# Kernel optimization log

Measured on AMD Instinct MI355X. Metric: run time of the kernel, lower is better.

Reference implementation:

```python
import jax, jax.numpy as jnp
import numpy as np

BS, N, D, H = 4, 2048, 512, 8
DK = D // H
XAVIER_STD = float(np.sqrt(2.0 / (D + D)))  # xavier_normal_, gain=1


def setup_inputs() -> dict:
    key = jax.random.key(0)
    ks = jax.random.split(key, 10)
    Q = jax.random.normal(ks[0], (BS, N, D), jnp.float32)
    K = jax.random.normal(ks[1], (BS, N, D), jnp.float32)
    V = jax.random.normal(ks[2], (BS, N, D), jnp.float32)
    q_mas = jax.random.randint(ks[3], (BS, N, 1), 0, 2).astype(jnp.float32)
    k_mas = jax.random.randint(ks[4], (BS, N, 1), 0, 2).astype(jnp.float32)
    # 0/1 attention mask; force self-edges so no row is fully masked (avoids NaN softmax)
    att_mas = jax.random.randint(ks[5], (BS, N, N), 0, 2).astype(jnp.float32)
    att_mas = jnp.maximum(att_mas, jnp.eye(N, dtype=jnp.float32)[None])
    WQ = jax.random.normal(ks[6], (D, D), jnp.float32) * XAVIER_STD
    WK = jax.random.normal(ks[7], (D, D), jnp.float32) * XAVIER_STD
    WV = jax.random.normal(ks[8], (D, D), jnp.float32) * XAVIER_STD
    WO = jax.random.normal(ks[9], (D, D), jnp.float32) * XAVIER_STD
    return {"Q": Q, "K": K, "V": V, "q_mas": q_mas, "k_mas": k_mas,
            "att_mas": att_mas, "WQ": WQ, "WK": WK, "WV": WV, "WO": WO}


def reference(Q, K, V, q_mas, k_mas, att_mas, WQ, WK, WV, WO):
    bs, n, d = Q.shape
    h, dk = H, DK
    qm = q_mas.reshape(bs, 1, n, 1)  # (bs,1,n,1)
    km = k_mas.reshape(bs, 1, n, 1)
    # nn.Linear (no bias): x @ W.T ; split heads -> (bs,h,n,dk); apply pre-masks
    Qh = qm * (Q @ WQ.T).reshape(bs, n, h, dk).transpose(0, 2, 1, 3)
    Kh = km * (K @ WK.T).reshape(bs, n, h, dk).transpose(0, 2, 1, 3)
    Vh = km * (V @ WV.T).reshape(bs, n, h, dk).transpose(0, 2, 1, 3)
    scores = jnp.einsum('bhqd,bhkd->bhqk', Qh, Kh) / jnp.sqrt(jnp.float32(dk))
    mas = att_mas.reshape(bs, 1, n, n)
    scores = jnp.where(mas.astype(bool), scores, -jnp.inf)
    attn = jax.nn.softmax(scores, axis=-1) * mas
    y = jnp.einsum('bhqk,bhkd->bhqd', attn, Vh) * km  # post-mask (note: km over query dim, as in source)
    y = y.transpose(0, 2, 1, 3).reshape(bs, n, d)
    y = (y @ WO.T) * k_mas.reshape(bs, n, 1)
    return y
```

## Files before the change

kernel.cpp:

```cpp
#include <hip/hip_runtime.h>


#define BS_    4
#define NSEQ   2048
#define DMODEL 512
#define NH     8
#define DKH    64
#define MROWS  (BS_ * NSEQ)

typedef unsigned short ushort_t;
typedef __attribute__((ext_vector_type(8))) short short8;
typedef __attribute__((ext_vector_type(4))) float floatx4;

__device__ __forceinline__ ushort_t f2bf(float f) {
    unsigned int x = __builtin_bit_cast(unsigned int, f);
    unsigned int lsb = (x >> 16) & 1u;
    x += 0x7fffu + lsb;
    return (ushort_t)(x >> 16);
}
__device__ __forceinline__ floatx4 mfma_bf16(short8 a, short8 b, floatx4 c) {
    return __builtin_amdgcn_mfma_f32_16x16x32_bf16(a, b, c, 0, 0, 0);
}
__device__ __forceinline__ void gld16(const ushort_t* g, ushort_t* l) {
    __builtin_amdgcn_global_load_lds(
        (const __attribute__((address_space(1))) unsigned int*)g,
        (__attribute__((address_space(3))) unsigned int*)l, 16, 0, 0);
}

__global__ __launch_bounds__(256) void cvt3_kernel(const float* __restrict__ a,
                                                   const float* __restrict__ b,
                                                   const float* __restrict__ c,
                                                   ushort_t* __restrict__ dst, int n4) {
    const float* src = (blockIdx.y == 0) ? a : (blockIdx.y == 1) ? b : c;
    ushort_t* d = dst + (size_t)blockIdx.y * ((size_t)n4 * 4);
    const int i = blockIdx.x * blockDim.x + threadIdx.x;
    const float4 v = ((const float4*)src)[i];
    ushort4 o;
    o.x = f2bf(v.x); o.y = f2bf(v.y); o.z = f2bf(v.z); o.w = f2bf(v.w);
    ((ushort4*)d)[i] = o;
}

__global__ __launch_bounds__(256) void cvt4_kernel(const float* __restrict__ a,
                                                   const float* __restrict__ b,
                                                   const float* __restrict__ c,
                                                   const float* __restrict__ e,
                                                   ushort_t* __restrict__ dst, int n4) {
    const float* src = (blockIdx.y == 0) ? a : (blockIdx.y == 1) ? b
                     : (blockIdx.y == 2) ? c : e;
    ushort_t* d = dst + (size_t)blockIdx.y * ((size_t)n4 * 4);
    const int i = blockIdx.x * blockDim.x + threadIdx.x;
    const float4 v = ((const float4*)src)[i];
    ushort4 o;
    o.x = f2bf(v.x); o.y = f2bf(v.y); o.z = f2bf(v.z); o.w = f2bf(v.w);
    ((ushort4*)d)[i] = o;
}

__global__ __launch_bounds__(256) void gemm_proj(const ushort_t* __restrict__ Xall,
                                                 const ushort_t* __restrict__ Wall,
                                                 const float* __restrict__ qmas,
                                                 const float* __restrict__ kmas,
                                                 ushort_t* __restrict__ Qh,
                                                 ushort_t* __restrict__ Kh,
                                                 ushort_t* __restrict__ Vt) {
    __shared__ ushort_t As[128 * 32];
    __shared__ ushort_t Bs[128 * 32];
    const int z = blockIdx.z;
    const ushort_t* X  = Xall + (size_t)z * MROWS * DMODEL;
    const ushort_t* Wb = Wall + (size_t)z * DMODEL * DMODEL;
    const float* rowmask = (z == 0) ? qmas : kmas;

    const int tid  = threadIdx.x;
    const int wave = tid >> 6;
    const int lane = tid & 63;
    const int l16  = lane & 15;
    const int quad = lane >> 4;
    const int wr   = wave >> 1;
    const int wc   = wave & 1;
    const int m0   = blockIdx.x * 128;
    const int n0   = blockIdx.y * 128;
    const int crow = lane >> 2;
    const int koff = (lane & 3) * 8;

    floatx4 acc[4][4];
#pragma unroll
    for (int t = 0; t < 4; ++t)
#pragma unroll
        for (int u = 0; u < 4; ++u) acc[t][u] = (floatx4){0.f, 0.f, 0.f, 0.f};

    for (int k0 = 0; k0 < DMODEL; k0 += 32) {
#pragma unroll
        for (int c2 = 0; c2 < 2; ++c2) {
            const int c = wave * 2 + c2;
            gld16(X  + (size_t)(m0 + c * 16 + crow) * DMODEL + k0 + koff, &As[c * 512]);
            gld16(Wb + (size_t)(n0 + c * 16 + crow) * DMODEL + k0 + koff, &Bs[c * 512]);
        }
        __syncthreads();
        short8 a[4], b[4];
#pragma unroll
        for (int t = 0; t < 4; ++t)
            a[t] = *(const short8*)&As[(wr * 64 + t * 16 + l16) * 32 + quad * 8];
#pragma unroll
        for (int u = 0; u < 4; ++u)
            b[u] = *(const short8*)&Bs[(wc * 64 + u * 16 + l16) * 32 + quad * 8];
#pragma unroll
        for (int t = 0; t < 4; ++t)
#pragma unroll
            for (int u = 0; u < 4; ++u) acc[t][u] = mfma_bf16(a[t], b[u], acc[t][u]);
        __syncthreads();
    }

    float rm[4][4];
#pragma unroll
    for (int t = 0; t < 4; ++t)
#pragma unroll
        for (int r = 0; r < 4; ++r)
            rm[t][r] = rowmask[m0 + wr * 64 + t * 16 + quad * 4 + r];

    const int bb    = m0 >> 11;
    const int nbase = (m0 & (NSEQ - 1)) + wr * 64;
#pragma unroll
    for (int t = 0; t < 4; ++t) {
#pragma unroll
        for (int u = 0; u < 4; ++u) {
            const int d = n0 + wc * 64 + u * 16 + l16;
            const int h = d >> 6, cc = d & 63;
            if (z < 2) {
                ushort_t* dst = (z == 0) ? Qh : Kh;
#pragma unroll
                for (int r = 0; r < 4; ++r) {
                    const int n = nbase + t * 16 + quad * 4 + r;
                    dst[((size_t)(bb * NH + h) * NSEQ + n) * DKH + cc] =
                        f2bf(acc[t][u][r] * rm[t][r]);
                }
            } else {
                ushort4 pk;
                pk.x = f2bf(acc[t][u][0] * rm[t][0]);
                pk.y = f2bf(acc[t][u][1] * rm[t][1]);
                pk.z = f2bf(acc[t][u][2] * rm[t][2]);
                pk.w = f2bf(acc[t][u][3] * rm[t][3]);
                const int n = nbase + t * 16 + quad * 4;
                *(ushort4*)(Vt + ((size_t)(bb * NH + h) * DKH + cc) * NSEQ + n) = pk;
            }
        }
    }
}

__global__ __launch_bounds__(256) void gemm_out(const ushort_t* __restrict__ X,
                                                const ushort_t* __restrict__ Wb,
                                                const float* __restrict__ rowmask,
                                                float* __restrict__ dst) {
    __shared__ ushort_t As[128 * 32];
    __shared__ ushort_t Bs[128 * 32];
    const int tid  = threadIdx.x;
    const int wave = tid >> 6;
    const int lane = tid & 63;
    const int l16  = lane & 15;
    const int quad = lane >> 4;
    const int wr   = wave >> 1;
    const int wc   = wave & 1;
    const int m0   = blockIdx.x * 128;
    const int n0   = blockIdx.y * 128;
    const int crow = lane >> 2;
    const int koff = (lane & 3) * 8;

    floatx4 acc[4][4];
#pragma unroll
    for (int t = 0; t < 4; ++t)
#pragma unroll
        for (int u = 0; u < 4; ++u) acc[t][u] = (floatx4){0.f, 0.f, 0.f, 0.f};

    for (int k0 = 0; k0 < DMODEL; k0 += 32) {
#pragma unroll
        for (int c2 = 0; c2 < 2; ++c2) {
            const int c = wave * 2 + c2;
            gld16(X  + (size_t)(m0 + c * 16 + crow) * DMODEL + k0 + koff, &As[c * 512]);
            gld16(Wb + (size_t)(n0 + c * 16 + crow) * DMODEL + k0 + koff, &Bs[c * 512]);
        }
        __syncthreads();
        short8 a[4], b[4];
#pragma unroll
        for (int t = 0; t < 4; ++t)
            a[t] = *(const short8*)&As[(wr * 64 + t * 16 + l16) * 32 + quad * 8];
#pragma unroll
        for (int u = 0; u < 4; ++u)
            b[u] = *(const short8*)&Bs[(wc * 64 + u * 16 + l16) * 32 + quad * 8];
#pragma unroll
        for (int t = 0; t < 4; ++t)
#pragma unroll
            for (int u = 0; u < 4; ++u) acc[t][u] = mfma_bf16(a[t], b[u], acc[t][u]);
        __syncthreads();
    }

#pragma unroll
    for (int t = 0; t < 4; ++t) {
#pragma unroll
        for (int r = 0; r < 4; ++r) {
            const int m = m0 + wr * 64 + t * 16 + quad * 4 + r;
            const float rm = rowmask[m];
#pragma unroll
            for (int u = 0; u < 4; ++u) {
                const int d = n0 + wc * 64 + u * 16 + l16;
                dst[(size_t)m * DMODEL + d] = acc[t][u][r] * rm;
            }
        }
    }
}

__global__ __launch_bounds__(256) void attn_kernel(const ushort_t* __restrict__ Qh,
                                                   const ushort_t* __restrict__ Kh,
                                                   const ushort_t* __restrict__ Vt,
                                                   const float* __restrict__ amas,
                                                   const float* __restrict__ kmas,
                                                   ushort_t* __restrict__ y) {
    __shared__ __align__(16) ushort_t Ks[128 * 72];
    __shared__ __align__(16) ushort_t Vs[64 * 136];
    __shared__ __align__(16) ushort_t Ps[4][16 * 136];

    const int tid  = threadIdx.x;
    const int wave = tid >> 6;
    const int lane = tid & 63;
    const int l16  = lane & 15;
    const int quad = lane >> 4;
    const int h    = blockIdx.y;
    const int b    = blockIdx.z;
    const int qw   = blockIdx.x * 64 + wave * 16;

    const ushort_t* Kb = Kh + (size_t)(b * NH + h) * NSEQ * DKH;
    const ushort_t* Vb = Vt + (size_t)(b * NH + h) * DKH * NSEQ;
    const float*    Am = amas + (size_t)(b * NSEQ + qw) * NSEQ;

    const ushort_t* Qp = Qh + ((size_t)((b * NH + h) * NSEQ) + qw + l16) * DKH + quad * 8;
    const short8 qfa = *(const short8*)Qp;
    const short8 qfb = *(const short8*)(Qp + 32);

    float lpart[4] = {0.f, 0.f, 0.f, 0.f};
    floatx4 accO[4];
#pragma unroll
    for (int ct = 0; ct < 4; ++ct) accO[ct] = (floatx4){0.f, 0.f, 0.f, 0.f};

    const float CEXP = 0.18033688011112042f;

    for (int kt = 0; kt < NSEQ / 128; ++kt) {
        const int k0 = kt * 128;

        short8 kv[4], vv[4];
#pragma unroll
        for (int i = 0; i < 4; ++i) {
            const int c = tid + i * 256;
            kv[i] = *(const short8*)(Kb + (size_t)(k0 + (c >> 3)) * DKH + (c & 7) * 8);
        }
#pragma unroll
        for (int i = 0; i < 4; ++i) {
            const int c = tid + i * 256;
            vv[i] = *(const short8*)(Vb + (size_t)(c >> 4) * NSEQ + k0 + (c & 15) * 8);
        }
        float av[8][4];
#pragma unroll
        for (int fr = 0; fr < 8; ++fr)
#pragma unroll
            for (int r = 0; r < 4; ++r)
                av[fr][r] = Am[(size_t)(quad * 4 + r) * NSEQ + k0 + fr * 16 + l16];

        __syncthreads();
#pragma unroll
        for (int i = 0; i < 4; ++i) {
            const int c = tid + i * 256;
            *(short8*)&Ks[(c >> 3) * 72 + (c & 7) * 8] = kv[i];
        }
#pragma unroll
        for (int i = 0; i < 4; ++i) {
            const int c = tid + i * 256;
            *(short8*)&Vs[(c >> 4) * 136 + (c & 15) * 8] = vv[i];
        }
        __syncthreads();

        floatx4 S[8];
#pragma unroll
        for (int fr = 0; fr < 8; ++fr) {
            const short8 ka = *(const short8*)&Ks[(fr * 16 + l16) * 72 + quad * 8];
            const short8 kb = *(const short8*)&Ks[(fr * 16 + l16) * 72 + 32 + quad * 8];
            floatx4 s = {0.f, 0.f, 0.f, 0.f};
            s = mfma_bf16(qfa, ka, s);
            s = mfma_bf16(qfb, kb, s);
            S[fr] = s;
        }

#pragma unroll
        for (int fr = 0; fr < 8; ++fr) {
#pragma unroll
            for (int r = 0; r < 4; ++r) {
                const float p = av[fr][r] * exp2f(S[fr][r] * CEXP);
                lpart[r] += p;
                Ps[wave][(quad * 4 + r) * 136 + fr * 16 + l16] = f2bf(p);
            }
        }

        __builtin_amdgcn_wave_barrier();
        short8 pf[4];
#pragma unroll
        for (int kf = 0; kf < 4; ++kf)
            pf[kf] = *(const short8*)&Ps[wave][l16 * 136 + kf * 32 + quad * 8];
        __builtin_amdgcn_wave_barrier();

#pragma unroll
        for (int ct = 0; ct < 4; ++ct) {
#pragma unroll
            for (int kf = 0; kf < 4; ++kf) {
                const short8 vb = *(const short8*)&Vs[(ct * 16 + l16) * 136 + kf * 32 + quad * 8];
                accO[ct] = mfma_bf16(pf[kf], vb, accO[ct]);
            }
        }
    }

#pragma unroll
    for (int r = 0; r < 4; ++r) {
        float l = lpart[r];
        l += __shfl_xor(l, 1);
        l += __shfl_xor(l, 2);
        l += __shfl_xor(l, 4);
        l += __shfl_xor(l, 8);
        const int q = qw + quad * 4 + r;
        const float scale = kmas[b * NSEQ + q] / l;
#pragma unroll
        for (int ct = 0; ct < 4; ++ct) {
            y[(size_t)(b * NSEQ + q) * DMODEL + h * DKH + ct * 16 + l16] =
                f2bf(accO[ct][r] * scale);
        }
    }
}

extern "C" void kernel_launch(void* const* d_in, const int* in_sizes, int n_in,
                              void* d_out, int out_size, void* d_ws, size_t ws_size,
                              hipStream_t stream) {
    (void)in_sizes; (void)n_in; (void)out_size; (void)ws_size;
    const float* Q  = (const float*)d_in[0];
    const float* K  = (const float*)d_in[1];
    const float* V  = (const float*)d_in[2];
    const float* qm = (const float*)d_in[3];
    const float* km = (const float*)d_in[4];
    const float* am = (const float*)d_in[5];
    const float* WQ = (const float*)d_in[6];
    const float* WK = (const float*)d_in[7];
    const float* WV = (const float*)d_in[8];
    const float* WO = (const float*)d_in[9];

    const size_t XN = (size_t)MROWS * DMODEL;
    const size_t WN = (size_t)DMODEL * DMODEL;
    ushort_t* Xbf = (ushort_t*)d_ws;
    ushort_t* Wbf = Xbf + 3 * XN;
    ushort_t* WOb = Wbf + 3 * WN;
    ushort_t* Qh  = Wbf + 4 * WN;
    ushort_t* Kh  = Qh + XN;
    ushort_t* Vt  = Kh + XN;
    ushort_t* y   = Vt + XN;
    float* out = (float*)d_out;

    hipLaunchKernelGGL(cvt3_kernel, dim3(4096, 3), dim3(256), 0, stream,
                       Q, K, V, Xbf, (int)(XN / 4));
    hipLaunchKernelGGL(cvt4_kernel, dim3(256, 4), dim3(256), 0, stream,
                       WQ, WK, WV, WO, Wbf, (int)(WN / 4));

    hipLaunchKernelGGL(gemm_proj, dim3(MROWS / 128, DMODEL / 128, 3), dim3(256), 0, stream,
                       Xbf, Wbf, qm, km, Qh, Kh, Vt);

    hipLaunchKernelGGL(attn_kernel, dim3(NSEQ / 64, NH, BS_), dim3(256), 0, stream,
                       Qh, Kh, Vt, am, km, y);

    hipLaunchKernelGGL(gemm_out, dim3(MROWS / 128, DMODEL / 128), dim3(256), 0, stream,
                       y, WOb, km, out);
}
```

Measured before the change: 288.4 us.

## Use direct-to-LDS loads in attention, read weights from global, widen GEMM K-step

The projection and output GEMMs now step K by 64 and stage only the activation tile in shared memory via global_load_lds, while each wave reads its weight fragments straight from global memory into registers. The attention kernel replaces register-staged K/V copies with direct global-to-LDS loads into unpadded 32-wide subtiles, re-lays out the P buffer to match, and sets a launch-bounds occupancy hint of 3. The bf16 conversion drops round-to-nearest-even tie handling for a cheaper round-half-up. These changes aim to cut LDS traffic, VGPR staging and barrier overhead, but unpadded LDS rows risk bank conflicts, and uncoalesced weight loads may add global latency.

```diff
diff --git a/kernel.cpp b/kernel.cpp
--- a/kernel.cpp
+++ b/kernel.cpp
@@ -14,9 +14,7 @@
 
 __device__ __forceinline__ ushort_t f2bf(float f) {
     unsigned int x = __builtin_bit_cast(unsigned int, f);
-    unsigned int lsb = (x >> 16) & 1u;
-    x += 0x7fffu + lsb;
-    return (ushort_t)(x >> 16);
+    return (ushort_t)((x + 0x8000u) >> 16);
 }
 __device__ __forceinline__ floatx4 mfma_bf16(short8 a, short8 b, floatx4 c) {
     return __builtin_amdgcn_mfma_f32_16x16x32_bf16(a, b, c, 0, 0, 0);
@@ -62,8 +60,7 @@
                                                  ushort_t* __restrict__ Qh,
                                                  ushort_t* __restrict__ Kh,
                                                  ushort_t* __restrict__ Vt) {
-    __shared__ ushort_t As[128 * 32];
-    __shared__ ushort_t Bs[128 * 32];
+    __shared__ ushort_t As[2][128 * 32];
     const int z = blockIdx.z;
     const ushort_t* X  = Xall + (size_t)z * MROWS * DMODEL;
     const ushort_t* Wb = Wall + (size_t)z * DMODEL * DMODEL;
@@ -78,8 +75,8 @@
     const int wc   = wave & 1;
     const int m0   = blockIdx.x * 128;
     const int n0   = blockIdx.y * 128;
-    const int crow = lane >> 2;
-    const int koff = (lane & 3) * 8;
+    const int r4   = lane >> 2;
+    const int p4   = lane & 3;
 
     floatx4 acc[4][4];
 #pragma unroll
@@ -87,25 +84,39 @@
 #pragma unroll
         for (int u = 0; u < 4; ++u) acc[t][u] = (floatx4){0.f, 0.f, 0.f, 0.f};
 
-    for (int k0 = 0; k0 < DMODEL; k0 += 32) {
-#pragma unroll
-        for (int c2 = 0; c2 < 2; ++c2) {
-            const int c = wave * 2 + c2;
-            gld16(X  + (size_t)(m0 + c * 16 + crow) * DMODEL + k0 + koff, &As[c * 512]);
-            gld16(Wb + (size_t)(n0 + c * 16 + crow) * DMODEL + k0 + koff, &Bs[c * 512]);
-        }
-        __syncthreads();
-        short8 a[4], b[4];
+    const ushort_t* Wrow[4];
+#pragma unroll
+    for (int u = 0; u < 4; ++u)
+        Wrow[u] = Wb + (size_t)(n0 + wc * 64 + u * 16 + l16) * DMODEL + quad * 8;
+
+    for (int k0 = 0; k0 < DMODEL; k0 += 64) {
+#pragma unroll
+        for (int i = 0; i < 4; ++i) {
+            const int idx = wave * 4 + i;
+            const int h = idx >> 3, rg = idx & 7;
+            gld16(X + (size_t)(m0 + rg * 16 + r4) * DMODEL + k0 + h * 32 + p4 * 8,
+                  &As[h][rg * 512]);
+        }
+        short8 bf[4][2];
+#pragma unroll
+        for (int u = 0; u < 4; ++u)
+#pragma unroll
+            for (int kc = 0; kc < 2; ++kc)
+                bf[u][kc] = *(const short8*)(Wrow[u] + k0 + kc * 32);
+        __syncthreads();
+        short8 af[4][2];
 #pragma unroll
         for (int t = 0; t < 4; ++t)
-            a[t] = *(const short8*)&As[(wr * 64 + t * 16 + l16) * 32 + quad * 8];
-#pragma unroll
-        for (int u = 0; u < 4; ++u)
-            b[u] = *(const short8*)&Bs[(wc * 64 + u * 16 + l16) * 32 + quad * 8];
+#pragma unroll
+            for (int kc = 0; kc < 2; ++kc)
+                af[t][kc] = *(const short8*)&As[kc][(wr * 64 + t * 16 + l16) * 32 + quad * 8];
 #pragma unroll
         for (int t = 0; t < 4; ++t)
 #pragma unroll
-            for (int u = 0; u < 4; ++u) acc[t][u] = mfma_bf16(a[t], b[u], acc[t][u]);
+            for (int u = 0; u < 4; ++u) {
+                acc[t][u] = mfma_bf16(af[t][0], bf[u][0], acc[t][u]);
+                acc[t][u] = mfma_bf16(af[t][1], bf[u][1], acc[t][u]);
+            }
         __syncthreads();
     }
 
@@ -149,8 +160,7 @@
                                                 const ushort_t* __restrict__ Wb,
                                                 const float* __restrict__ rowmask,
                                                 float* __restrict__ dst) {
-    __shared__ ushort_t As[128 * 32];
-    __shared__ ushort_t Bs[128 * 32];
+    __shared__ ushort_t As[2][128 * 32];
     const int tid  = threadIdx.x;
     const int wave = tid >> 6;
     const int lane = tid & 63;
@@ -160,8 +170,8 @@
     const int wc   = wave & 1;
     const int m0   = blockIdx.x * 128;
     const int n0   = blockIdx.y * 128;
-    const int crow = lane >> 2;
-    const int koff = (lane & 3) * 8;
+    const int r4   = lane >> 2;
+    const int p4   = lane & 3;
 
     floatx4 acc[4][4];
 #pragma unroll
@@ -169,25 +179,39 @@
 #pragma unroll
         for (int u = 0; u < 4; ++u) acc[t][u] = (floatx4){0.f, 0.f, 0.f, 0.f};
 
-    for (int k0 = 0; k0 < DMODEL; k0 += 32) {
-#pragma unroll
-        for (int c2 = 0; c2 < 2; ++c2) {
-            const int c = wave * 2 + c2;
-            gld16(X  + (size_t)(m0 + c * 16 + crow) * DMODEL + k0 + koff, &As[c * 512]);
-            gld16(Wb + (size_t)(n0 + c * 16 + crow) * DMODEL + k0 + koff, &Bs[c * 512]);
-        }
-        __syncthreads();
-        short8 a[4], b[4];
+    const ushort_t* Wrow[4];
+#pragma unroll
+    for (int u = 0; u < 4; ++u)
+        Wrow[u] = Wb + (size_t)(n0 + wc * 64 + u * 16 + l16) * DMODEL + quad * 8;
+
+    for (int k0 = 0; k0 < DMODEL; k0 += 64) {
+#pragma unroll
+        for (int i = 0; i < 4; ++i) {
+            const int idx = wave * 4 + i;
+            const int h = idx >> 3, rg = idx & 7;
+            gld16(X + (size_t)(m0 + rg * 16 + r4) * DMODEL + k0 + h * 32 + p4 * 8,
+                  &As[h][rg * 512]);
+        }
+        short8 bf[4][2];
+#pragma unroll
+        for (int u = 0; u < 4; ++u)
+#pragma unroll
+            for (int kc = 0; kc < 2; ++kc)
+                bf[u][kc] = *(const short8*)(Wrow[u] + k0 + kc * 32);
+        __syncthreads();
+        short8 af[4][2];
 #pragma unroll
         for (int t = 0; t < 4; ++t)
-            a[t] = *(const short8*)&As[(wr * 64 + t * 16 + l16) * 32 + quad * 8];
-#pragma unroll
-        for (int u = 0; u < 4; ++u)
-            b[u] = *(const short8*)&Bs[(wc * 64 + u * 16 + l16) * 32 + quad * 8];
+#pragma unroll
+            for (int kc = 0; kc < 2; ++kc)
+                af[t][kc] = *(const short8*)&As[kc][(wr * 64 + t * 16 + l16) * 32 + quad * 8];
 #pragma unroll
         for (int t = 0; t < 4; ++t)
 #pragma unroll
-            for (int u = 0; u < 4; ++u) acc[t][u] = mfma_bf16(a[t], b[u], acc[t][u]);
+            for (int u = 0; u < 4; ++u) {
+                acc[t][u] = mfma_bf16(af[t][0], bf[u][0], acc[t][u]);
+                acc[t][u] = mfma_bf16(af[t][1], bf[u][1], acc[t][u]);
+            }
         __syncthreads();
     }
 
@@ -206,21 +230,23 @@
     }
 }
 
-__global__ __launch_bounds__(256) void attn_kernel(const ushort_t* __restrict__ Qh,
-                                                   const ushort_t* __restrict__ Kh,
-                                                   const ushort_t* __restrict__ Vt,
-                                                   const float* __restrict__ amas,
-                                                   const float* __restrict__ kmas,
-                                                   ushort_t* __restrict__ y) {
-    __shared__ __align__(16) ushort_t Ks[128 * 72];
-    __shared__ __align__(16) ushort_t Vs[64 * 136];
-    __shared__ __align__(16) ushort_t Ps[4][16 * 136];
+__global__ __launch_bounds__(256, 3) void attn_kernel(const ushort_t* __restrict__ Qh,
+                                                      const ushort_t* __restrict__ Kh,
+                                                      const ushort_t* __restrict__ Vt,
+                                                      const float* __restrict__ amas,
+                                                      const float* __restrict__ kmas,
+                                                      ushort_t* __restrict__ y) {
+    __shared__ ushort_t Ks[2][128 * 32];
+    __shared__ ushort_t Vs[4][64 * 32];
+    __shared__ ushort_t Ps[4][4][16 * 32];
 
     const int tid  = threadIdx.x;
     const int wave = tid >> 6;
     const int lane = tid & 63;
     const int l16  = lane & 15;
     const int quad = lane >> 4;
+    const int r4   = lane >> 2;
+    const int p4   = lane & 3;
     const int h    = blockIdx.y;
     const int b    = blockIdx.z;
     const int qw   = blockIdx.x * 64 + wave * 16;
@@ -243,17 +269,8 @@
     for (int kt = 0; kt < NSEQ / 128; ++kt) {
         const int k0 = kt * 128;
 
-        short8 kv[4], vv[4];
-#pragma unroll
-        for (int i = 0; i < 4; ++i) {
-            const int c = tid + i * 256;
-            kv[i] = *(const short8*)(Kb + (size_t)(k0 + (c >> 3)) * DKH + (c & 7) * 8);
-        }
-#pragma unroll
-        for (int i = 0; i < 4; ++i) {
-            const int c = tid + i * 256;
-            vv[i] = *(const short8*)(Vb + (size_t)(c >> 4) * NSEQ + k0 + (c & 15) * 8);
-        }
+        __syncthreads();
+
         float av[8][4];
 #pragma unroll
         for (int fr = 0; fr < 8; ++fr)
@@ -261,24 +278,27 @@
             for (int r = 0; r < 4; ++r)
                 av[fr][r] = Am[(size_t)(quad * 4 + r) * NSEQ + k0 + fr * 16 + l16];
 
-        __syncthreads();
 #pragma unroll
         for (int i = 0; i < 4; ++i) {
-            const int c = tid + i * 256;
-            *(short8*)&Ks[(c >> 3) * 72 + (c & 7) * 8] = kv[i];
+            const int idx = wave * 4 + i;
+            const int hh = idx >> 3, rg = idx & 7;
+            gld16(Kb + (size_t)(k0 + rg * 16 + r4) * DKH + hh * 32 + p4 * 8,
+                  &Ks[hh][rg * 512]);
         }
 #pragma unroll
         for (int i = 0; i < 4; ++i) {
-            const int c = tid + i * 256;
-            *(short8*)&Vs[(c >> 4) * 136 + (c & 15) * 8] = vv[i];
+            const int idx = wave * 4 + i;
+            const int kf = idx >> 2, rg = idx & 3;
+            gld16(Vb + (size_t)(rg * 16 + r4) * NSEQ + k0 + kf * 32 + p4 * 8,
+                  &Vs[kf][rg * 512]);
         }
         __syncthreads();
 
         floatx4 S[8];
 #pragma unroll
         for (int fr = 0; fr < 8; ++fr) {
-            const short8 ka = *(const short8*)&Ks[(fr * 16 + l16) * 72 + quad * 8];
-            const short8 kb = *(const short8*)&Ks[(fr * 16 + l16) * 72 + 32 + quad * 8];
+            const short8 ka = *(const short8*)&Ks[0][(fr * 16 + l16) * 32 + quad * 8];
+            const short8 kb = *(const short8*)&Ks[1][(fr * 16 + l16) * 32 + quad * 8];
             floatx4 s = {0.f, 0.f, 0.f, 0.f};
             s = mfma_bf16(qfa, ka, s);
             s = mfma_bf16(qfb, kb, s);
@@ -291,7 +311,7 @@
             for (int r = 0; r < 4; ++r) {
                 const float p = av[fr][r] * exp2f(S[fr][r] * CEXP);
                 lpart[r] += p;
-                Ps[wave][(quad * 4 + r) * 136 + fr * 16 + l16] = f2bf(p);
+                Ps[wave][fr >> 1][(quad * 4 + r) * 32 + (fr & 1) * 16 + l16] = f2bf(p);
             }
         }
 
@@ -299,14 +319,14 @@
         short8 pf[4];
 #pragma unroll
         for (int kf = 0; kf < 4; ++kf)
-            pf[kf] = *(const short8*)&Ps[wave][l16 * 136 + kf * 32 + quad * 8];
+            pf[kf] = *(const short8*)&Ps[wave][kf][l16 * 32 + quad * 8];
         __builtin_amdgcn_wave_barrier();
 
 #pragma unroll
         for (int ct = 0; ct < 4; ++ct) {
 #pragma unroll
             for (int kf = 0; kf < 4; ++kf) {
-                const short8 vb = *(const short8*)&Vs[(ct * 16 + l16) * 136 + kf * 32 + quad * 8];
+                const short8 vb = *(const short8*)&Vs[kf][(ct * 16 + l16) * 32 + quad * 8];
                 accO[ct] = mfma_bf16(pf[kf], vb, accO[ct]);
             }
         }
```

Result: slower. 294.2 us (+2.0%).
